# Kernel optimization log

Measured on AMD Instinct MI355X. Metric: run time of the kernel, lower is better.

The kernel has to match this reference:

```python
import jax, jax.numpy as jnp
import numpy as np

# --- constants matching ElectrostaticEnergy defaults ---
KE = 14.399645351950548
KEHALF = KE / 2.0
CUTON = 2.5
CUTOFF = 7.5
LR_CUTOFF = 10.0
CUTON16 = CUTON ** 16
CUT_RCONSTANT = LR_CUTOFF ** 15 / (LR_CUTOFF ** 16 + CUTON ** 16) ** (17.0 / 16.0)
CUT_CONSTANT = 1.0 / (CUTON ** 16 + LR_CUTOFF ** 16) ** (1.0 / 16.0) + LR_CUTOFF ** 16 / (LR_CUTOFF ** 16 + CUTON ** 16) ** (17.0 / 16.0)

N_ATOMS = 102400   # total atoms
N_PAIRS = N_ATOMS * 64  # 6,553,600 edges
N_MOL = 2048       # molecules (atoms per molecule = 50)


def switch_function(x):
    """SpookyNet-style smooth switch: 1 below cuton, 0 above cutoff."""
    t = (CUTOFF - x) / (CUTOFF - CUTON)

    def comp(u):
        u_safe = jnp.where(u <= 0, jnp.ones_like(u), u)
        return jnp.where(u <= 0, jnp.zeros_like(u), jnp.exp(-1.0 / u_safe))

    fp = comp(t)
    fm = comp(1.0 - t)
    return jnp.where(t <= 0, jnp.zeros_like(t),
                     jnp.where(t >= 1, jnp.ones_like(t), fp / (fp + fm)))


def setup_inputs() -> dict:
    key = jax.random.key(0)
    k1, k2, k3, k4, k5 = jax.random.split(key, 5)
    atomic_numbers = jax.random.randint(k1, (N_ATOMS,), 1, 10, dtype=jnp.int32)
    q = 0.1 * jax.random.normal(k2, (N_ATOMS,), dtype=jnp.float32)  # partial charges
    # uniform components in [0.8, 6.5] -> d_ij roughly in [1.4, 11.2], spans all cutoffs
    r_ij = jax.random.uniform(k3, (N_PAIRS, 3), dtype=jnp.float32, minval=0.8, maxval=6.5)
    idx_i = jax.random.randint(k4, (N_PAIRS,), 0, N_ATOMS, dtype=jnp.int32)
    idx_j = jax.random.randint(k5, (N_PAIRS,), 0, N_ATOMS, dtype=jnp.int32)
    idx_m = jnp.repeat(jnp.arange(N_MOL, dtype=jnp.int32), N_ATOMS // N_MOL)  # sorted atom->mol map
    return {"atomic_numbers": atomic_numbers, "q": q, "r_ij": r_ij,
            "idx_i": idx_i, "idx_j": idx_j, "idx_m": idx_m, "maxm": N_MOL}


def reference(atomic_numbers, q, r_ij, idx_i, idx_j, idx_m, maxm):
    N = q.shape[0]
    d_ij = jnp.linalg.norm(r_ij, axis=1)                      # [P]
    fac = KEHALF * q[idx_i] * q[idx_j]                        # [P] gather
    f = switch_function(d_ij)                                 # [P]
    # lr_cutoff branch of the original module
    x_coulomb = 1.0 / d_ij + d_ij / (LR_CUTOFF ** 2) - 2.0 / LR_CUTOFF
    coulomb = jnp.where(d_ij < LR_CUTOFF, x_coulomb, jnp.zeros_like(d_ij))
    damped = (d_ij ** 16 + CUTON16) ** (-1.0 / 16.0) + (1.0 - f) * CUT_RCONSTANT * d_ij - CUT_CONSTANT
    e_edge = fac * (f * damped + (1.0 - f) * coulomb)         # [P]
    y_atom = jax.ops.segment_sum(e_edge, idx_i, num_segments=N)        # edge -> atom
    y = jax.ops.segment_sum(y_atom, idx_m, num_segments=maxm)          # atom -> molecule
    return y  # [maxm]
```

## Files before the change

### kernel.cpp

```cpp
#include <hip/hip_runtime.h>
#include <math.h>

#define NMOL   2048
#define APM    50u
#define BLOCK  512
#define GRID   2048

typedef float __attribute__((ext_vector_type(4))) fx4;
typedef int   __attribute__((ext_vector_type(4))) ix4;

#define KEHALF_F   7.199822675975274f
#define CUTON16_F  2328306.4365386963f
#define CUT_RCONST 0.01f
#define CUT_CONST  0.2f

__global__ void zero_y_kernel(float* __restrict__ y, int n) {
    int i = blockIdx.x * blockDim.x + threadIdx.x;
    if (i < n) y[i] = 0.0f;
}

__device__ __forceinline__ float edge_energy(float x, float yv, float z,
                                             float qi, float qj) {
    const float d   = sqrtf(fmaf(x, x, fmaf(yv, yv, z * z)));
    const float fac = KEHALF_F * qi * qj;

    const float t  = fminf(fmaxf((7.5f - d) * 0.2f, 0.0f), 1.0f);
    const float fp = __expf(-__builtin_amdgcn_rcpf(t));
    const float fm = __expf(-__builtin_amdgcn_rcpf(1.0f - t));
    const float f  = fp * __builtin_amdgcn_rcpf(fp + fm);

    const float invd = __builtin_amdgcn_rcpf(d);
    const float coul = (d < 10.0f) ? fmaf(d, 0.01f, invd - 0.2f) : 0.0f;

    const float d2 = d * d, d4 = d2 * d2, d8 = d4 * d4, d16 = d8 * d8;
    const float damped = __expf(-0.0625f * __logf(d16 + CUTON16_F))
                       + (1.0f - f) * (CUT_RCONST * d) - CUT_CONST;

    return fac * (f * damped + (1.0f - f) * coul);
}

template<int USE_PART>
__launch_bounds__(BLOCK, 6)
__global__ void edge_energy_kernel(const float* __restrict__ q,
                                   const float* __restrict__ r,
                                   const int*   __restrict__ idx_i,
                                   const int*   __restrict__ idx_j,
                                   float*       __restrict__ out,
                                   int P)
{
    __shared__ float bins[NMOL];
    for (int b = threadIdx.x; b < NMOL; b += BLOCK) bins[b] = 0.0f;
    __syncthreads();

    const int ngroups = P >> 2;
    const int GB      = GRID * BLOCK;
    const fx4* r4  = (const fx4*)r;
    const ix4* i4p = (const ix4*)idx_i;
    const ix4* j4p = (const ix4*)idx_j;

    for (int g = blockIdx.x * BLOCK + threadIdx.x; g < ngroups; g += 2 * GB) {
        const int  g2r  = g + GB;
        const bool has2 = g2r < ngroups;
        const int  g2   = has2 ? g2r : g;

        const fx4 ra1 = __builtin_nontemporal_load(&r4[3 * g  + 0]);
        const fx4 rb1 = __builtin_nontemporal_load(&r4[3 * g  + 1]);
        const fx4 rc1 = __builtin_nontemporal_load(&r4[3 * g  + 2]);
        const ix4 ii1 = __builtin_nontemporal_load(&i4p[g]);
        const ix4 jj1 = __builtin_nontemporal_load(&j4p[g]);
        const fx4 ra2 = __builtin_nontemporal_load(&r4[3 * g2 + 0]);
        const fx4 rb2 = __builtin_nontemporal_load(&r4[3 * g2 + 1]);
        const fx4 rc2 = __builtin_nontemporal_load(&r4[3 * g2 + 2]);
        const ix4 ii2 = __builtin_nontemporal_load(&i4p[g2]);
        const ix4 jj2 = __builtin_nontemporal_load(&j4p[g2]);

        const float qi10 = q[ii1.x], qj10 = q[jj1.x];
        const float qi11 = q[ii1.y], qj11 = q[jj1.y];
        const float qi12 = q[ii1.z], qj12 = q[jj1.z];
        const float qi13 = q[ii1.w], qj13 = q[jj1.w];
        const float qi20 = q[ii2.x], qj20 = q[jj2.x];
        const float qi21 = q[ii2.y], qj21 = q[jj2.y];
        const float qi22 = q[ii2.z], qj22 = q[jj2.z];
        const float qi23 = q[ii2.w], qj23 = q[jj2.w];

        const float e10 = edge_energy(ra1.x, ra1.y, ra1.z, qi10, qj10);
        const float e11 = edge_energy(ra1.w, rb1.x, rb1.y, qi11, qj11);
        const float e12 = edge_energy(rb1.z, rb1.w, rc1.x, qi12, qj12);
        const float e13 = edge_energy(rc1.y, rc1.z, rc1.w, qi13, qj13);

        atomicAdd(&bins[(unsigned)ii1.x / APM], e10);
        atomicAdd(&bins[(unsigned)ii1.y / APM], e11);
        atomicAdd(&bins[(unsigned)ii1.z / APM], e12);
        atomicAdd(&bins[(unsigned)ii1.w / APM], e13);

        const float e20 = edge_energy(ra2.x, ra2.y, ra2.z, qi20, qj20);
        const float e21 = edge_energy(ra2.w, rb2.x, rb2.y, qi21, qj21);
        const float e22 = edge_energy(rb2.z, rb2.w, rc2.x, qi22, qj22);
        const float e23 = edge_energy(rc2.y, rc2.z, rc2.w, qi23, qj23);

        if (has2) {
            atomicAdd(&bins[(unsigned)ii2.x / APM], e20);
            atomicAdd(&bins[(unsigned)ii2.y / APM], e21);
            atomicAdd(&bins[(unsigned)ii2.z / APM], e22);
            atomicAdd(&bins[(unsigned)ii2.w / APM], e23);
        }
    }

    for (int p = ((P >> 2) << 2) + blockIdx.x * BLOCK + threadIdx.x; p < P;
         p += GB) {
        const float e = edge_energy(r[3 * p], r[3 * p + 1], r[3 * p + 2],
                                    q[idx_i[p]], q[idx_j[p]]);
        atomicAdd(&bins[(unsigned)idx_i[p] / APM], e);
    }

    __syncthreads();
    if (USE_PART) {
        fx4* prow = (fx4*)(out + (size_t)blockIdx.x * NMOL);
        const fx4* b4 = (const fx4*)bins;
        const int t = threadIdx.x;
        __builtin_nontemporal_store(b4[t], &prow[t]);
    } else {
        const int off = (blockIdx.x * 97) & (NMOL - 1);
        for (int b0 = threadIdx.x; b0 < NMOL; b0 += BLOCK) {
            const int b = (b0 + off) & (NMOL - 1);
            unsafeAtomicAdd(&out[b], bins[b]);
        }
    }
}

__launch_bounds__(1024, 2)
__global__ void reduce_kernel(const float* __restrict__ part,
                              float*       __restrict__ y)
{
    const int tid  = threadIdx.x;
    const int w    = tid >> 6;
    const int lane = tid & 63;
    const int rr   = lane >> 4;
    const int c    = lane & 15;
    const int b0   = blockIdx.x * 64;

    const fx4* p4 = (const fx4*)part;
    fx4 acc = {0.0f, 0.0f, 0.0f, 0.0f};
    int row = w * 128 + rr;
    #pragma unroll 4
    for (int k = 0; k < 32; ++k) {
        acc += p4[(size_t)row * 512 + (b0 >> 2) + c];
        row += 4;
    }
    acc.x += __shfl_xor(acc.x, 16, 64); acc.y += __shfl_xor(acc.y, 16, 64);
    acc.z += __shfl_xor(acc.z, 16, 64); acc.w += __shfl_xor(acc.w, 16, 64);
    acc.x += __shfl_xor(acc.x, 32, 64); acc.y += __shfl_xor(acc.y, 32, 64);
    acc.z += __shfl_xor(acc.z, 32, 64); acc.w += __shfl_xor(acc.w, 32, 64);

    __shared__ float red[16][64];
    if (rr == 0) {
        red[w][4 * c + 0] = acc.x; red[w][4 * c + 1] = acc.y;
        red[w][4 * c + 2] = acc.z; red[w][4 * c + 3] = acc.w;
    }
    __syncthreads();
    if (tid < 64) {
        float v = 0.0f;
        #pragma unroll
        for (int ww = 0; ww < 16; ++ww) v += red[ww][tid];
        y[b0 + tid] = v;
    }
}

extern "C" void kernel_launch(void* const* d_in, const int* in_sizes, int n_in,
                              void* d_out, int out_size, void* d_ws, size_t ws_size,
                              hipStream_t stream) {
    const float* q     = (const float*)d_in[1];
    const float* r_ij  = (const float*)d_in[2];
    const int*   idx_i = (const int*)d_in[3];
    const int*   idx_j = (const int*)d_in[4];
    float*       y     = (float*)d_out;
    const int P = in_sizes[3];

    const size_t part_bytes = (size_t)GRID * NMOL * sizeof(float);
    const bool use_part = ws_size >= part_bytes;

    zero_y_kernel<<<(out_size + 255) / 256, 256, 0, stream>>>(y, out_size);
    if (use_part) {
        float* part = (float*)d_ws;
        edge_energy_kernel<1><<<GRID, BLOCK, 0, stream>>>(q, r_ij, idx_i, idx_j,
                                                          part, P);
        reduce_kernel<<<NMOL / 64, 1024, 0, stream>>>(part, y);
    } else {
        edge_energy_kernel<0><<<GRID, BLOCK, 0, stream>>>(q, r_ij, idx_i, idx_j,
                                                          y, P);
    }
}
```

Measured before the change: 226.6 us.

## Replace per-block partial rows with four replicated atomic accumulators

Instead of writing a full 2048-bin partial row per block to workspace (16 MB) and reducing it with a separate kernel, each block now atomically adds its shared-memory bins into one of four replicated global accumulators, selected by block index. A small final kernel then sums the four replicas. This removes a large write and read of partials in exchange for global atomic contention, spread across four copies and staggered offsets. It also drops the fallback path and assumes the workspace is large enough for the replicas.

```diff
diff --git a/kernel.cpp b/kernel.cpp
--- a/kernel.cpp
+++ b/kernel.cpp
@@ -5,6 +5,7 @@
 #define APM    50u
 #define BLOCK  512
 #define GRID   2048
+#define NREP   4
 
 typedef float __attribute__((ext_vector_type(4))) fx4;
 typedef int   __attribute__((ext_vector_type(4))) ix4;
@@ -14,9 +15,9 @@
 #define CUT_RCONST 0.01f
 #define CUT_CONST  0.2f
 
-__global__ void zero_y_kernel(float* __restrict__ y, int n) {
+__global__ void zero_rep_kernel(float* __restrict__ rep) {
     int i = blockIdx.x * blockDim.x + threadIdx.x;
-    if (i < n) y[i] = 0.0f;
+    if (i < NREP * NMOL) rep[i] = 0.0f;
 }
 
 __device__ __forceinline__ float edge_energy(float x, float yv, float z,
@@ -39,13 +40,12 @@
     return fac * (f * damped + (1.0f - f) * coul);
 }
 
-template<int USE_PART>
 __launch_bounds__(BLOCK, 6)
 __global__ void edge_energy_kernel(const float* __restrict__ q,
                                    const float* __restrict__ r,
                                    const int*   __restrict__ idx_i,
                                    const int*   __restrict__ idx_j,
-                                   float*       __restrict__ out,
+                                   float*       __restrict__ rep,
                                    int P)
 {
     __shared__ float bins[NMOL];
@@ -114,55 +114,22 @@
     }
 
     __syncthreads();
-    if (USE_PART) {
-        fx4* prow = (fx4*)(out + (size_t)blockIdx.x * NMOL);
-        const fx4* b4 = (const fx4*)bins;
-        const int t = threadIdx.x;
-        __builtin_nontemporal_store(b4[t], &prow[t]);
-    } else {
-        const int off = (blockIdx.x * 97) & (NMOL - 1);
-        for (int b0 = threadIdx.x; b0 < NMOL; b0 += BLOCK) {
-            const int b = (b0 + off) & (NMOL - 1);
-            unsafeAtomicAdd(&out[b], bins[b]);
-        }
+    float* yr = rep + (size_t)(blockIdx.x & (NREP - 1)) * NMOL;
+    const int off = ((blockIdx.x >> 2) * 97) & (NMOL - 1);
+    for (int b0 = threadIdx.x; b0 < NMOL; b0 += BLOCK) {
+        const int b = (b0 + off) & (NMOL - 1);
+        unsafeAtomicAdd(&yr[b], bins[b]);
     }
 }
 
-__launch_bounds__(1024, 2)
-__global__ void reduce_kernel(const float* __restrict__ part,
-                              float*       __restrict__ y)
-{
-    const int tid  = threadIdx.x;
-    const int w    = tid >> 6;
-    const int lane = tid & 63;
-    const int rr   = lane >> 4;
-    const int c    = lane & 15;
-    const int b0   = blockIdx.x * 64;
-
-    const fx4* p4 = (const fx4*)part;
-    fx4 acc = {0.0f, 0.0f, 0.0f, 0.0f};
-    int row = w * 128 + rr;
-    #pragma unroll 4
-    for (int k = 0; k < 32; ++k) {
-        acc += p4[(size_t)row * 512 + (b0 >> 2) + c];
-        row += 4;
-    }
-    acc.x += __shfl_xor(acc.x, 16, 64); acc.y += __shfl_xor(acc.y, 16, 64);
-    acc.z += __shfl_xor(acc.z, 16, 64); acc.w += __shfl_xor(acc.w, 16, 64);
-    acc.x += __shfl_xor(acc.x, 32, 64); acc.y += __shfl_xor(acc.y, 32, 64);
-    acc.z += __shfl_xor(acc.z, 32, 64); acc.w += __shfl_xor(acc.w, 32, 64);
-
-    __shared__ float red[16][64];
-    if (rr == 0) {
-        red[w][4 * c + 0] = acc.x; red[w][4 * c + 1] = acc.y;
-        red[w][4 * c + 2] = acc.z; red[w][4 * c + 3] = acc.w;
-    }
-    __syncthreads();
-    if (tid < 64) {
+__global__ void final_kernel(const float* __restrict__ rep,
+                             float*       __restrict__ y) {
+    const int b = blockIdx.x * blockDim.x + threadIdx.x;
+    if (b < NMOL) {
         float v = 0.0f;
         #pragma unroll
-        for (int ww = 0; ww < 16; ++ww) v += red[ww][tid];
-        y[b0 + tid] = v;
+        for (int k = 0; k < NREP; ++k) v += rep[k * NMOL + b];
+        y[b] = v;
     }
 }
 
@@ -174,19 +141,10 @@
     const int*   idx_i = (const int*)d_in[3];
     const int*   idx_j = (const int*)d_in[4];
     float*       y     = (float*)d_out;
+    float*       rep   = (float*)d_ws;
     const int P = in_sizes[3];
 
-    const size_t part_bytes = (size_t)GRID * NMOL * sizeof(float);
-    const bool use_part = ws_size >= part_bytes;
-
-    zero_y_kernel<<<(out_size + 255) / 256, 256, 0, stream>>>(y, out_size);
-    if (use_part) {
-        float* part = (float*)d_ws;
-        edge_energy_kernel<1><<<GRID, BLOCK, 0, stream>>>(q, r_ij, idx_i, idx_j,
-                                                          part, P);
-        reduce_kernel<<<NMOL / 64, 1024, 0, stream>>>(part, y);
-    } else {
-        edge_energy_kernel<0><<<GRID, BLOCK, 0, stream>>>(q, r_ij, idx_i, idx_j,
-                                                          y, P);
-    }
+    zero_rep_kernel<<<(NREP * NMOL + 255) / 256, 256, 0, stream>>>(rep);
+    edge_energy_kernel<<<GRID, BLOCK, 0, stream>>>(q, r_ij, idx_i, idx_j, rep, P);
+    final_kernel<<<(NMOL + 255) / 256, 256, 0, stream>>>(rep, y);
 }
```

Measured after the change: 212.8 us. 6.1% less time.
